# Optimization experiments

Measured on AMD Instinct MI355X. Metric: run time of the kernel, lower is better.

Reference implementation:

```python
import jax, jax.numpy as jnp
import numpy as np

B, S, D, H, E, K = 2, 1024, 768, 12, 8, 2
DF = 4 * D
HD = D // H
EPS = 1e-5

def layer_norm(x, g, b):
    m = jnp.mean(x, axis=-1, keepdims=True)
    v = jnp.mean(jnp.square(x - m), axis=-1, keepdims=True)
    return (x - m) * jax.lax.rsqrt(v + EPS) * g + b

def setup_inputs() -> dict:
    key = jax.random.key(0)
    ks = jax.random.split(key, 16)
    s = lambda i, shape, sc: jax.random.normal(ks[i], shape, jnp.float32) * sc
    return {
        'x': s(0, (B, S, D), 1.0),
        'ln1_g': jnp.ones((D,), jnp.float32), 'ln1_b': jnp.zeros((D,), jnp.float32),
        'Wq': s(1, (D, D), 0.02), 'Wk': s(2, (D, D), 0.02), 'Wv': s(3, (D, D), 0.02),
        'Wo': s(4, (D, D), 0.02), 'bo': jnp.zeros((D,), jnp.float32),
        'ln2_g': jnp.ones((D,), jnp.float32), 'ln2_b': jnp.zeros((D,), jnp.float32),
        'Wr': s(5, (D, E), 0.02), 'br': jnp.zeros((E,), jnp.float32),
        'W1': s(6, (E, D, DF), 0.02), 'b1': jnp.zeros((E, DF), jnp.float32),
        'W2': s(7, (E, DF, D), 0.02), 'b2': jnp.zeros((E, D), jnp.float32),
    }

def _attn(xn, Wq, Wk, Wv, Wo, bo):
    # xn: [B,S,D]
    q = (xn @ Wq).reshape(B, S, H, HD).transpose(0, 2, 1, 3)
    k = (xn @ Wk).reshape(B, S, H, HD).transpose(0, 2, 1, 3)
    v = (xn @ Wv).reshape(B, S, H, HD).transpose(0, 2, 1, 3)
    scores = jnp.einsum('bhqd,bhkd->bhqk', q, k) / jnp.sqrt(jnp.float32(HD))
    causal = jnp.tril(jnp.ones((S, S), bool))
    scores = jnp.where(causal, scores, jnp.float32(-1e9))
    w = jax.nn.softmax(scores, axis=-1)
    out = jnp.einsum('bhqk,bhkd->bhqd', w, v)
    out = out.transpose(0, 2, 1, 3).reshape(B, S, D)
    return out @ Wo + bo

def _smoe(xn, Wr, br, W1, b1, W2, b2):
    logits = xn @ Wr + br                               # [B,S,E]
    topv, topi = jax.lax.top_k(logits, K)               # [B,S,K]
    gw = jax.nn.softmax(topv, axis=-1)                  # softmax over selected experts
    oh = jax.nn.one_hot(topi, E, dtype=xn.dtype)        # [B,S,K,E]
    gate = jnp.einsum('bske,bsk->bse', oh, gw)          # sparse gate, zeros elsewhere
    h = jax.nn.gelu(jnp.einsum('bsd,edf->bsef', xn, W1) + b1, approximate=False)
    eo = jnp.einsum('bsef,efd->bsed', h, W2) + b2       # [B,S,E,D]
    return jnp.einsum('bsed,bse->bsd', eo, gate)

def reference(x, ln1_g, ln1_b, Wq, Wk, Wv, Wo, bo, ln2_g, ln2_b, Wr, br, W1, b1, W2, b2):
    h = x + _attn(layer_norm(x, ln1_g, ln1_b), Wq, Wk, Wv, Wo, bo)
    out = h + _smoe(layer_norm(h, ln2_g, ln2_b), Wr, br, W1, b1, W2, b2)
    return out
```

## Files before the change

### kernel.cpp

```cpp
#include <hip/hip_runtime.h>

using bf16x8 = __attribute__((ext_vector_type(8))) short;
using f32x4  = __attribute__((ext_vector_type(4))) float;

#define DEV __device__ __forceinline__

DEV short f2bf(float x){
  unsigned u = __float_as_uint(x);
  u += 0x7fffu + ((u >> 16) & 1u);
  return (short)(u >> 16);
}
DEV float bf2f(short h){ return __uint_as_float(((unsigned)(unsigned short)h) << 16); }

#define MFMA16(a,b,c) __builtin_amdgcn_mfma_f32_16x16x32_bf16(a,b,c,0,0,0)

DEV void gl_lds16(const void* g, void* l){
  __builtin_amdgcn_global_load_lds(
      (const __attribute__((address_space(1))) unsigned*)g,
      (__attribute__((address_space(3))) unsigned*)l, 16, 0, 0);
}


__global__ void k_transpose(const float* __restrict__ src, long sbatch,
                            short* __restrict__ dhi, short* __restrict__ dlo, long dbatch,
                            int R, int C){
  __shared__ float tile[32][33];
  const float* s = src + (long)blockIdx.z * sbatch;
  int c0 = blockIdx.x * 32, r0 = blockIdx.y * 32;
  int tx = threadIdx.x & 31, ty = threadIdx.x >> 5;
  #pragma unroll
  for (int i = 0; i < 4; i++)
    tile[ty + 8*i][tx] = s[(long)(r0 + ty + 8*i) * C + c0 + tx];
  __syncthreads();
  #pragma unroll
  for (int i = 0; i < 4; i++){
    int c = c0 + ty + 8*i;
    float v = tile[tx][ty + 8*i];
    short hv = f2bf(v);
    long o = (long)blockIdx.z * dbatch + (long)c * R + r0 + tx;
    dhi[o] = hv;
    if (dlo) dlo[o] = f2bf(v - bf2f(hv));
  }
}

__global__ void k_ln1(const float* __restrict__ x, const float* __restrict__ g,
                      const float* __restrict__ bb,
                      short* __restrict__ xh, short* __restrict__ xl){
  int t = blockIdx.x, tid = threadIdx.x;
  const float* xr = x + (long)t * 768;
  float v[3];
  #pragma unroll
  for (int j = 0; j < 3; j++) v[j] = xr[tid + 256*j];
  float s = v[0]+v[1]+v[2];
  float q = v[0]*v[0]+v[1]*v[1]+v[2]*v[2];
  #pragma unroll
  for (int o = 32; o > 0; o >>= 1){ s += __shfl_down(s,o,64); q += __shfl_down(q,o,64); }
  __shared__ float ss[4], qs[4];
  int w = tid >> 6;
  if ((tid & 63) == 0){ ss[w] = s; qs[w] = q; }
  __syncthreads();
  float St = ss[0]+ss[1]+ss[2]+ss[3], Qt = qs[0]+qs[1]+qs[2]+qs[3];
  float mean = St * (1.f/768.f);
  float var  = Qt * (1.f/768.f) - mean*mean;
  float inv  = 1.f / sqrtf(var + 1e-5f);
  #pragma unroll
  for (int j = 0; j < 3; j++){
    int d = tid + 256*j;
    float xn = (v[j]-mean)*inv*g[d] + bb[d];
    short hv = f2bf(xn);
    xh[(long)t*768 + d] = hv;
    xl[(long)t*768 + d] = f2bf(xn - bf2f(hv));
  }
}

__global__ __launch_bounds__(256,2) void k_qkv(
    const short* __restrict__ Ah, const short* __restrict__ Al,
    const short* __restrict__ Bh, const short* __restrict__ Bl,
    short* __restrict__ qh, short* __restrict__ ql,
    short* __restrict__ kh, short* __restrict__ kl,
    short* __restrict__ vh, short* __restrict__ vl){
  int M0 = blockIdx.x * 128, N0 = blockIdx.y * 128;
  __shared__ __align__(16) short lah[128*64], lal[128*64], lbh[128*64], lbl[128*64];
  int tid = threadIdx.x;
  int w = tid >> 6, lane = tid & 63, l15 = lane & 15, quad = lane >> 4;
  int mbase = (w & 1) * 64, nbase = (w >> 1) * 64;
  f32x4 acc[4][4];
  #pragma unroll
  for (int i = 0; i < 4; i++)
    #pragma unroll
    for (int j = 0; j < 4; j++) acc[i][j] = (f32x4){0.f,0.f,0.f,0.f};
  int rl = lane >> 3, pch = lane & 7;
  long gA[4], gB[4];
  #pragma unroll
  for (int j = 0; j < 4; j++){
    int r = w*32 + j*8 + rl;
    int c = pch ^ (r & 7);
    gA[j] = (long)(M0 + r)*768 + c*8;
    gB[j] = (long)(N0 + r)*768 + c*8;
  }
  for (int k0 = 0; k0 < 768; k0 += 64){
    #pragma unroll
    for (int j = 0; j < 4; j++){
      gl_lds16(Ah + gA[j] + k0, lah + w*2048 + j*512);
      gl_lds16(Al + gA[j] + k0, lal + w*2048 + j*512);
      gl_lds16(Bh + gB[j] + k0, lbh + w*2048 + j*512);
      gl_lds16(Bl + gB[j] + k0, lbl + w*2048 + j*512);
    }
    __syncthreads();
    #pragma unroll
    for (int kk = 0; kk < 2; kk++){
      int swq = ((kk*4 + quad) ^ (l15 & 7)) * 8;
      bf16x8 afh[4], afl[4];
      #pragma unroll
      for (int mt = 0; mt < 4; mt++){
        afh[mt] = *(const bf16x8*)&lah[(mbase+mt*16+l15)*64 + swq];
        afl[mt] = *(const bf16x8*)&lal[(mbase+mt*16+l15)*64 + swq];
      }
      #pragma unroll
      for (int nt = 0; nt < 4; nt++){
        bf16x8 bfh = *(const bf16x8*)&lbh[(nbase+nt*16+l15)*64 + swq];
        bf16x8 bfl = *(const bf16x8*)&lbl[(nbase+nt*16+l15)*64 + swq];
        #pragma unroll
        for (int mt = 0; mt < 4; mt++){
          acc[mt][nt] = MFMA16(afh[mt], bfh, acc[mt][nt]);
          acc[mt][nt] = MFMA16(afh[mt], bfl, acc[mt][nt]);
          acc[mt][nt] = MFMA16(afl[mt], bfh, acc[mt][nt]);
        }
      }
    }
    __syncthreads();
  }
  #pragma unroll
  for (int mt = 0; mt < 4; mt++){
    #pragma unroll
    for (int nt = 0; nt < 4; nt++){
      #pragma unroll
      for (int rg = 0; rg < 4; rg++){
        int m = M0 + mbase + mt*16 + quad*4 + rg;
        int n = N0 + nbase + nt*16 + l15;
        float vv = acc[mt][nt][rg];
        int bi = m >> 10, si = m & 1023;
        if (n < 768){
          float sv = vv * 0.125f;
          short hv = f2bf(sv);
          int hh = n >> 6, hd = n & 63;
          long o = (((long)(bi*12+hh)*1024) + si)*64 + hd;
          qh[o] = hv; ql[o] = f2bf(sv - bf2f(hv));
        } else if (n < 1536){
          int n2 = n - 768;
          short hv = f2bf(vv);
          int hh = n2 >> 6, hd = n2 & 63;
          long o = (((long)(bi*12+hh)*1024) + si)*64 + hd;
          kh[o] = hv; kl[o] = f2bf(vv - bf2f(hv));
        } else {
          int n2 = n - 1536;
          short hv = f2bf(vv);
          int hh = n2 >> 6, hd = n2 & 63;
          long o = (((long)(bi*12+hh)*64) + hd)*1024 + si;
          vh[o] = hv; vl[o] = f2bf(vv - bf2f(hv));
        }
      }
    }
  }
}

__global__ __launch_bounds__(256,3) void k_attn(
    const short* __restrict__ qh, const short* __restrict__ ql,
    const short* __restrict__ kh, const short* __restrict__ kl,
    const short* __restrict__ vth, const short* __restrict__ vtl,
    float* __restrict__ po, float* __restrict__ pm, float* __restrict__ pl){
  int qt = blockIdx.x >> 1, half = blockIdx.x & 1, bh = blockIdx.y;
  int q0 = qt * 64;
  long base = (long)bh * 1024 * 64;
  int ktb = half ? ((qt + 2) >> 1) : 0;
  int kte = half ? (qt + 1) : ((qt + 2) >> 1);
  __shared__ __align__(16) short skh[64*64], skl[64*64], svh[64*64], svl[64*64];
  __shared__ __align__(16) short sph[4][16*72], spl[4][16*72];
  int tid = threadIdx.x, w = tid >> 6, lane = tid & 63, l15 = lane & 15, quad = lane >> 4;
  bf16x8 qfh[2], qfl[2];
  #pragma unroll
  for (int c = 0; c < 2; c++){
    long qa = base + (long)(q0 + w*16 + l15)*64 + c*32 + quad*8;
    qfh[c] = *(const bf16x8*)(qh + qa);
    qfl[c] = *(const bf16x8*)(ql + qa);
  }
  f32x4 oacc[4];
  #pragma unroll
  for (int i = 0; i < 4; i++) oacc[i] = (f32x4){0.f,0.f,0.f,0.f};
  float m_i[4] = {-1e30f,-1e30f,-1e30f,-1e30f};
  float l_i[4] = {0.f,0.f,0.f,0.f};
  const short* gsrc = (w==0) ? kh : (w==1) ? kl : (w==2) ? vth : vtl;
  short* myb = (w==0) ? skh : (w==1) ? skl : (w==2) ? svh : svl;
  bool isv = (w >= 2);
  int rloc = lane >> 3, pch = lane & 7;
  for (int kt = ktb; kt < kte; kt++){
    #pragma unroll
    for (int j = 0; j < 8; j++){
      int r = j*8 + rloc;
      int c = pch ^ (r & 7);
      long ga = isv ? (base + (long)r*1024 + kt*64 + c*8)
                    : (base + (long)(kt*64 + r)*64 + c*8);
      gl_lds16(gsrc + ga, myb + j*512);
    }
    __syncthreads();
    f32x4 sfr[4];
    #pragma unroll
    for (int nt = 0; nt < 4; nt++){
      f32x4 c = (f32x4){0.f,0.f,0.f,0.f};
      int krow = (nt*16 + l15) * 64;
      #pragma unroll
      for (int ch = 0; ch < 2; ch++){
        int pc = ((ch*4 + quad) ^ (l15 & 7)) * 8;
        bf16x8 kfh = *(const bf16x8*)&skh[krow + pc];
        bf16x8 kfl = *(const bf16x8*)&skl[krow + pc];
        c = MFMA16(qfh[ch], kfh, c);
        c = MFMA16(qfh[ch], kfl, c);
        c = MFMA16(qfl[ch], kfh, c);
      }
      sfr[nt] = c;
    }
    if (kt == qt){
      #pragma unroll
      for (int nt = 0; nt < 4; nt++)
        #pragma unroll
        for (int rg = 0; rg < 4; rg++){
          int kp = nt*16 + l15, qp = w*16 + quad*4 + rg;
          if (kp > qp) sfr[nt][rg] = -1e30f;
        }
    }
    float rmax[4];
    #pragma unroll
    for (int rg = 0; rg < 4; rg++)
      rmax[rg] = fmaxf(fmaxf(sfr[0][rg], sfr[1][rg]), fmaxf(sfr[2][rg], sfr[3][rg]));
    #pragma unroll
    for (int xm = 1; xm < 16; xm <<= 1)
      #pragma unroll
      for (int rg = 0; rg < 4; rg++)
        rmax[rg] = fmaxf(rmax[rg], __shfl_xor(rmax[rg], xm, 64));
    float alpha[4];
    #pragma unroll
    for (int rg = 0; rg < 4; rg++){
      float mn = fmaxf(m_i[rg], rmax[rg]);
      alpha[rg] = expf(m_i[rg] - mn);
      m_i[rg] = mn;
    }
    float rsum[4] = {0.f,0.f,0.f,0.f};
    #pragma unroll
    for (int nt = 0; nt < 4; nt++)
      #pragma unroll
      for (int rg = 0; rg < 4; rg++){
        float p = expf(sfr[nt][rg] - m_i[rg]);
        sfr[nt][rg] = p; rsum[rg] += p;
      }
    #pragma unroll
    for (int xm = 1; xm < 16; xm <<= 1)
      #pragma unroll
      for (int rg = 0; rg < 4; rg++)
        rsum[rg] += __shfl_xor(rsum[rg], xm, 64);
    #pragma unroll
    for (int rg = 0; rg < 4; rg++) l_i[rg] = l_i[rg]*alpha[rg] + rsum[rg];
    #pragma unroll
    for (int hd = 0; hd < 4; hd++)
      #pragma unroll
      for (int rg = 0; rg < 4; rg++) oacc[hd][rg] *= alpha[rg];
    #pragma unroll
    for (int nt = 0; nt < 4; nt++)
      #pragma unroll
      for (int rg = 0; rg < 4; rg++){
        float p = sfr[nt][rg];
        short hv = f2bf(p);
        sph[w][(quad*4+rg)*72 + nt*16 + l15] = hv;
        spl[w][(quad*4+rg)*72 + nt*16 + l15] = f2bf(p - bf2f(hv));
      }
    bf16x8 pfh[2], pfl[2];
    #pragma unroll
    for (int ch = 0; ch < 2; ch++){
      pfh[ch] = *(const bf16x8*)&sph[w][l15*72 + ch*32 + quad*8];
      pfl[ch] = *(const bf16x8*)&spl[w][l15*72 + ch*32 + quad*8];
    }
    #pragma unroll
    for (int hd = 0; hd < 4; hd++){
      int vrow = (hd*16 + l15) * 64;
      #pragma unroll
      for (int ch = 0; ch < 2; ch++){
        int pc = ((ch*4 + quad) ^ (l15 & 7)) * 8;
        bf16x8 vfh = *(const bf16x8*)&svh[vrow + pc];
        bf16x8 vfl = *(const bf16x8*)&svl[vrow + pc];
        oacc[hd] = MFMA16(pfh[ch], vfh, oacc[hd]);
        oacc[hd] = MFMA16(pfh[ch], vfl, oacc[hd]);
        oacc[hd] = MFMA16(pfl[ch], vfh, oacc[hd]);
      }
    }
    __syncthreads();
  }
  long pb = ((long)(half*24 + bh)*1024);
  #pragma unroll
  for (int hdt = 0; hdt < 4; hdt++)
    #pragma unroll
    for (int rg = 0; rg < 4; rg++){
      int qp = q0 + w*16 + quad*4 + rg;
      po[(pb + qp)*64 + hdt*16 + l15] = oacc[hdt][rg];
    }
  if (l15 == 0){
    #pragma unroll
    for (int rg = 0; rg < 4; rg++){
      int qp = q0 + w*16 + quad*4 + rg;
      pm[pb + qp] = m_i[rg];
      pl[pb + qp] = l_i[rg];
    }
  }
}

__global__ void k_attn_combine(const float* __restrict__ po, const float* __restrict__ pm,
                               const float* __restrict__ pl,
                               short* __restrict__ oh, short* __restrict__ ol){
  int bh = blockIdx.y, tid = threadIdx.x;
  int r = blockIdx.x*64 + (tid >> 2);
  int c0 = (tid & 3) * 16;
  long i0 = (long)bh*1024 + r;
  long i1 = (long)(24 + bh)*1024 + r;
  float m0 = pm[i0], m1 = pm[i1], l0 = pl[i0], l1 = pl[i1];
  float m = fmaxf(m0, m1);
  float a0 = expf(m0 - m), a1 = expf(m1 - m);
  float inv = 1.f / (a0*l0 + a1*l1);
  a0 *= inv; a1 *= inv;
  int b = bh / 12, hh = bh % 12;
  long ob = ((long)(b*1024 + r))*768 + hh*64 + c0;
  short hv[16], lv[16];
  #pragma unroll
  for (int j = 0; j < 4; j++){
    float4 o0 = *(const float4*)&po[i0*64 + c0 + j*4];
    float4 o1 = *(const float4*)&po[i1*64 + c0 + j*4];
    float vs[4] = {a0*o0.x + a1*o1.x, a0*o0.y + a1*o1.y,
                   a0*o0.z + a1*o1.z, a0*o0.w + a1*o1.w};
    #pragma unroll
    for (int q = 0; q < 4; q++){
      short h = f2bf(vs[q]);
      hv[j*4+q] = h; lv[j*4+q] = f2bf(vs[q] - bf2f(h));
    }
  }
  *(bf16x8*)(oh + ob)     = *(bf16x8*)&hv[0];
  *(bf16x8*)(oh + ob + 8) = *(bf16x8*)&hv[8];
  *(bf16x8*)(ol + ob)     = *(bf16x8*)&lv[0];
  *(bf16x8*)(ol + ob + 8) = *(bf16x8*)&lv[8];
}

__global__ __launch_bounds__(256,2) void k_wo(
    const short* __restrict__ Ah, const short* __restrict__ Al,
    const short* __restrict__ Bh, const short* __restrict__ Bl,
    const float* __restrict__ x, const float* __restrict__ bo,
    float* __restrict__ hout){
  int M0 = blockIdx.x * 128, N0 = blockIdx.y * 128;
  __shared__ __align__(16) short lah[128*64], lal[128*64], lbh[128*64], lbl[128*64];
  int tid = threadIdx.x;
  int w = tid >> 6, lane = tid & 63, l15 = lane & 15, quad = lane >> 4;
  int mbase = (w & 1) * 64, nbase = (w >> 1) * 64;
  f32x4 acc[4][4];
  #pragma unroll
  for (int i = 0; i < 4; i++)
    #pragma unroll
    for (int j = 0; j < 4; j++) acc[i][j] = (f32x4){0.f,0.f,0.f,0.f};
  int rl = lane >> 3, pch = lane & 7;
  long gA[4], gB[4];
  #pragma unroll
  for (int j = 0; j < 4; j++){
    int r = w*32 + j*8 + rl;
    int c = pch ^ (r & 7);
    gA[j] = (long)(M0 + r)*768 + c*8;
    gB[j] = (long)(N0 + r)*768 + c*8;
  }
  for (int k0 = 0; k0 < 768; k0 += 64){
    #pragma unroll
    for (int j = 0; j < 4; j++){
      gl_lds16(Ah + gA[j] + k0, lah + w*2048 + j*512);
      gl_lds16(Al + gA[j] + k0, lal + w*2048 + j*512);
      gl_lds16(Bh + gB[j] + k0, lbh + w*2048 + j*512);
      gl_lds16(Bl + gB[j] + k0, lbl + w*2048 + j*512);
    }
    __syncthreads();
    #pragma unroll
    for (int kk = 0; kk < 2; kk++){
      int swq = ((kk*4 + quad) ^ (l15 & 7)) * 8;
      bf16x8 afh[4], afl[4];
      #pragma unroll
      for (int mt = 0; mt < 4; mt++){
        afh[mt] = *(const bf16x8*)&lah[(mbase+mt*16+l15)*64 + swq];
        afl[mt] = *(const bf16x8*)&lal[(mbase+mt*16+l15)*64 + swq];
      }
      #pragma unroll
      for (int nt = 0; nt < 4; nt++){
        bf16x8 bfh = *(const bf16x8*)&lbh[(nbase+nt*16+l15)*64 + swq];
        bf16x8 bfl = *(const bf16x8*)&lbl[(nbase+nt*16+l15)*64 + swq];
        #pragma unroll
        for (int mt = 0; mt < 4; mt++){
          acc[mt][nt] = MFMA16(afh[mt], bfh, acc[mt][nt]);
          acc[mt][nt] = MFMA16(afh[mt], bfl, acc[mt][nt]);
          acc[mt][nt] = MFMA16(afl[mt], bfh, acc[mt][nt]);
        }
      }
    }
    __syncthreads();
  }
  #pragma unroll
  for (int mt = 0; mt < 4; mt++)
    #pragma unroll
    for (int nt = 0; nt < 4; nt++)
      #pragma unroll
      for (int rg = 0; rg < 4; rg++){
        int m = M0 + mbase + mt*16 + quad*4 + rg;
        int n = N0 + nbase + nt*16 + l15;
        hout[(long)m*768 + n] = acc[mt][nt][rg] + x[(long)m*768 + n] + bo[n];
      }
}

__global__ void k_ln2router(const float* __restrict__ h, const float* __restrict__ g,
                            const float* __restrict__ bb, const float* __restrict__ Wr,
                            const float* __restrict__ br, short* __restrict__ xn2,
                            int* __restrict__ sel, float* __restrict__ gw){
  int wv = (blockIdx.x*256 + threadIdx.x) >> 6;
  int lane = threadIdx.x & 63;
  #pragma unroll
  for (int rep = 0; rep < 2; rep++){
    int t = wv*2 + rep;
    const float* xr = h + (long)t * 768;
    float v[12];
    #pragma unroll
    for (int j = 0; j < 12; j++) v[j] = xr[lane + 64*j];
    float s = 0.f, q = 0.f;
    #pragma unroll
    for (int j = 0; j < 12; j++){ s += v[j]; q += v[j]*v[j]; }
    #pragma unroll
    for (int xm = 1; xm < 64; xm <<= 1){ s += __shfl_xor(s, xm, 64); q += __shfl_xor(q, xm, 64); }
    float mean = s * (1.f/768.f);
    float var  = q * (1.f/768.f) - mean*mean;
    float inv  = 1.f / sqrtf(var + 1e-5f);
    float part[8] = {0,0,0,0,0,0,0,0};
    #pragma unroll
    for (int j = 0; j < 12; j++){
      int d = lane + 64*j;
      float xn = (v[j]-mean)*inv*g[d] + bb[d];
      xn2[(long)t*768 + d] = f2bf(xn);
      #pragma unroll
      for (int e = 0; e < 8; e++) part[e] += xn * Wr[d*8 + e];
    }
    #pragma unroll
    for (int xm = 1; xm < 64; xm <<= 1)
      #pragma unroll
      for (int e = 0; e < 8; e++) part[e] += __shfl_xor(part[e], xm, 64);
    if (lane == 0){
      float lg[8];
      #pragma unroll
      for (int e = 0; e < 8; e++) lg[e] = part[e] + br[e];
      int i1 = 0;
      for (int e = 1; e < 8; e++) if (lg[e] > lg[i1]) i1 = e;
      int i2 = -1;
      for (int e = 0; e < 8; e++){ if (e == i1) continue; if (i2 < 0 || lg[e] > lg[i2]) i2 = e; }
      float e2 = expf(lg[i2] - lg[i1]);
      float is = 1.f / (1.f + e2);
      gw[t*2]   = is;
      gw[t*2+1] = e2 * is;
      sel[t*2]   = i1;
      sel[t*2+1] = i2;
    }
  }
}

__global__ void k_build(const int* __restrict__ sel, int* __restrict__ poffs,
                        int* __restrict__ mbc, int* __restrict__ ptot,
                        int* __restrict__ pperm, int* __restrict__ inv){
  __shared__ int cnt8[8], cur[8];
  int tid = threadIdx.x;
  if (tid < 8) cnt8[tid] = 0;
  __syncthreads();
  #pragma unroll
  for (int r = 0; r < 4; r++) atomicAdd(&cnt8[sel[tid + r*1024]], 1);
  __syncthreads();
  if (tid == 0){
    int p = 0;
    for (int e = 0; e < 8; e++){
      cur[e] = p; poffs[e] = p;
      int pc = (cnt8[e] + 127) & ~127;
      mbc[e] = pc >> 7;
      p += pc;
    }
    *ptot = p;
  }
  __syncthreads();
  #pragma unroll
  for (int r = 0; r < 5; r++) pperm[tid + r*1024] = -1;
  __syncthreads();
  #pragma unroll
  for (int r = 0; r < 4; r++){
    int i = tid + r*1024;
    int pos = atomicAdd(&cur[sel[i]], 1);
    pperm[pos] = i;
    inv[i] = pos;
  }
}

__global__ __launch_bounds__(256,3) void k_moe1(
    const short* __restrict__ xn2, const short* __restrict__ W1T,
    const float* __restrict__ b1,
    const int* __restrict__ poffs, const int* __restrict__ mbc,
    const int* __restrict__ pperm, short* __restrict__ h1){
  int t = blockIdx.x;
  int e = t / 24, n = t % 24;
  if ((int)blockIdx.y >= mbc[e]) return;
  int M0 = poffs[e] + blockIdx.y * 128;
  int N0 = n * 128;
  const short* Bp = W1T + (long)e * 3072 * 768;
  __shared__ __align__(16) short la[128*64], lb[128*64];
  __shared__ int rtok[128];
  int tid = threadIdx.x, w = tid >> 6, lane = tid & 63, l15 = lane & 15, quad = lane >> 4;
  if (tid < 128) rtok[tid] = pperm[M0 + tid];
  __syncthreads();
  int rl = lane >> 3, pch = lane & 7;
  long gA[4], gB[4];
  #pragma unroll
  for (int j = 0; j < 4; j++){
    int r = w*32 + j*8 + rl;
    int c = pch ^ (r & 7);
    int tk = rtok[r]; tk = (tk >= 0) ? (tk >> 1) : 0;
    gA[j] = (long)tk*768 + c*8;
    gB[j] = (long)(N0 + r)*768 + c*8;
  }
  short* ldA = la + w*2048;
  short* ldB = lb + w*2048;
  f32x4 acc[4][4];
  #pragma unroll
  for (int i = 0; i < 4; i++)
    #pragma unroll
    for (int j = 0; j < 4; j++) acc[i][j] = (f32x4){0.f,0.f,0.f,0.f};
  int mbase = (w & 1) * 64, nbase = (w >> 1) * 64;
  for (int k0 = 0; k0 < 768; k0 += 64){
    #pragma unroll
    for (int j = 0; j < 4; j++) gl_lds16(xn2 + gA[j] + k0, ldA + j*512);
    #pragma unroll
    for (int j = 0; j < 4; j++) gl_lds16(Bp  + gB[j] + k0, ldB + j*512);
    __syncthreads();
    #pragma unroll
    for (int kk = 0; kk < 2; kk++){
      int swq = ((kk*4 + quad) ^ (l15 & 7)) * 8;
      bf16x8 af[4];
      #pragma unroll
      for (int mt = 0; mt < 4; mt++)
        af[mt] = *(const bf16x8*)&la[(mbase+mt*16+l15)*64 + swq];
      #pragma unroll
      for (int nt = 0; nt < 4; nt++){
        bf16x8 bf = *(const bf16x8*)&lb[(nbase+nt*16+l15)*64 + swq];
        #pragma unroll
        for (int mt = 0; mt < 4; mt++) acc[mt][nt] = MFMA16(af[mt], bf, acc[mt][nt]);
      }
    }
    __syncthreads();
  }
  #pragma unroll
  for (int mt = 0; mt < 4; mt++)
    #pragma unroll
    for (int nt = 0; nt < 4; nt++)
      #pragma unroll
      for (int rg = 0; rg < 4; rg++){
        int ml = mbase + mt*16 + quad*4 + rg;
        if (rtok[ml] >= 0){
          int nn = N0 + nbase + nt*16 + l15;
          float vv = acc[mt][nt][rg] + b1[e*3072 + nn];
          float gl = 0.5f * vv * (1.f + erff(vv * 0.70710678118654752f));
          h1[(long)(M0 + ml)*3072 + nn] = f2bf(gl);
        }
      }
}

__global__ __launch_bounds__(256,4) void k_moe2(
    const short* __restrict__ h1, const short* __restrict__ W2T,
    const float* __restrict__ b2,
    const int* __restrict__ poffs, const int* __restrict__ mbc,
    float* __restrict__ e0, float* __restrict__ e1,
    float* __restrict__ e2, float* __restrict__ e3){
  int t = blockIdx.x;
  int e = t / 24, r24 = t % 24;
  int n = r24 >> 2, ks = r24 & 3;
  if ((int)blockIdx.y >= mbc[e]) return;
  int M0 = poffs[e] + blockIdx.y * 128;
  int N0 = n * 128;
  int kbeg = ks * 768;
  const short* Bp = W2T + (long)e * 768 * 3072;
  float* eo = (ks == 0) ? e0 : (ks == 1) ? e1 : (ks == 2) ? e2 : e3;
  __shared__ __align__(16) short la[128*64], lb[128*64];
  int tid = threadIdx.x, w = tid >> 6, lane = tid & 63, l15 = lane & 15, quad = lane >> 4;
  int rl = lane >> 3, pch = lane & 7;
  long gA[4], gB[4];
  #pragma unroll
  for (int j = 0; j < 4; j++){
    int r = w*32 + j*8 + rl;
    int c = pch ^ (r & 7);
    gA[j] = (long)(M0 + r)*3072 + kbeg + c*8;
    gB[j] = (long)(N0 + r)*3072 + kbeg + c*8;
  }
  short* ldA = la + w*2048;
  short* ldB = lb + w*2048;
  f32x4 acc[4][4];
  #pragma unroll
  for (int i = 0; i < 4; i++)
    #pragma unroll
    for (int j = 0; j < 4; j++) acc[i][j] = (f32x4){0.f,0.f,0.f,0.f};
  int mbase = (w & 1) * 64, nbase = (w >> 1) * 64;
  for (int k0 = 0; k0 < 768; k0 += 64){
    #pragma unroll
    for (int j = 0; j < 4; j++) gl_lds16(h1 + gA[j] + k0, ldA + j*512);
    #pragma unroll
    for (int j = 0; j < 4; j++) gl_lds16(Bp + gB[j] + k0, ldB + j*512);
    __syncthreads();
    #pragma unroll
    for (int kk = 0; kk < 2; kk++){
      int swq = ((kk*4 + quad) ^ (l15 & 7)) * 8;
      bf16x8 af[4];
      #pragma unroll
      for (int mt = 0; mt < 4; mt++)
        af[mt] = *(const bf16x8*)&la[(mbase+mt*16+l15)*64 + swq];
      #pragma unroll
      for (int nt = 0; nt < 4; nt++){
        bf16x8 bf = *(const bf16x8*)&lb[(nbase+nt*16+l15)*64 + swq];
        #pragma unroll
        for (int mt = 0; mt < 4; mt++) acc[mt][nt] = MFMA16(af[mt], bf, acc[mt][nt]);
      }
    }
    __syncthreads();
  }
  #pragma unroll
  for (int mt = 0; mt < 4; mt++)
    #pragma unroll
    for (int nt = 0; nt < 4; nt++)
      #pragma unroll
      for (int rg = 0; rg < 4; rg++){
        int ml = mbase + mt*16 + quad*4 + rg;
        int nn = N0 + nbase + nt*16 + l15;
        float vv = acc[mt][nt][rg] + ((ks == 0) ? b2[e*768 + nn] : 0.f);
        eo[(long)(M0 + ml)*768 + nn] = vv;
      }
}

__global__ void k_combine(const float* __restrict__ h,
                          const float* __restrict__ e0, const float* __restrict__ e1,
                          const float* __restrict__ e2, const float* __restrict__ e3,
                          const int* __restrict__ inv, const float* __restrict__ gw,
                          float* __restrict__ out){
  int i = blockIdx.x * 256 + threadIdx.x;
  int t = i / 192, c = i - t * 192;
  int s0 = inv[2*t], s1 = inv[2*t+1];
  float g0 = gw[2*t], g1 = gw[2*t+1];
  float4 a  = ((const float4*)h)[i];
  long o0 = (long)s0*192 + c, o1 = (long)s1*192 + c;
  float4 x0 = ((const float4*)e0)[o0];
  float4 y0 = ((const float4*)e1)[o0];
  float4 z0 = ((const float4*)e2)[o0];
  float4 w0 = ((const float4*)e3)[o0];
  float4 x1 = ((const float4*)e0)[o1];
  float4 y1 = ((const float4*)e1)[o1];
  float4 z1 = ((const float4*)e2)[o1];
  float4 w1 = ((const float4*)e3)[o1];
  float4 o;
  o.x = a.x + g0*(x0.x + y0.x + z0.x + w0.x) + g1*(x1.x + y1.x + z1.x + w1.x);
  o.y = a.y + g0*(x0.y + y0.y + z0.y + w0.y) + g1*(x1.y + y1.y + z1.y + w1.y);
  o.z = a.z + g0*(x0.z + y0.z + z0.z + w0.z) + g1*(x1.z + y1.z + z1.z + w1.z);
  o.w = a.w + g0*(x0.w + y0.w + z0.w + w0.w) + g1*(x1.w + y1.w + z1.w + w1.w);
  ((float4*)out)[i] = o;
}

extern "C" void kernel_launch(void* const* d_in, const int* in_sizes, int n_in,
                              void* d_out, int out_size, void* d_ws, size_t ws_size,
                              hipStream_t stream){
  const float* x    = (const float*)d_in[0];
  const float* ln1g = (const float*)d_in[1];
  const float* ln1b = (const float*)d_in[2];
  const float* Wq   = (const float*)d_in[3];
  const float* Wk   = (const float*)d_in[4];
  const float* Wv   = (const float*)d_in[5];
  const float* Wo   = (const float*)d_in[6];
  const float* bo   = (const float*)d_in[7];
  const float* ln2g = (const float*)d_in[8];
  const float* ln2b = (const float*)d_in[9];
  const float* Wr   = (const float*)d_in[10];
  const float* br   = (const float*)d_in[11];
  const float* W1   = (const float*)d_in[12];
  const float* b1   = (const float*)d_in[13];
  const float* W2   = (const float*)d_in[14];
  const float* b2   = (const float*)d_in[15];

  char* ws = (char*)d_ws;
  size_t off = 0;
  auto alloc = [&](size_t bytes) -> void* {
    void* p = ws + off;
    off += (bytes + 255) & ~(size_t)255;
    return p;
  };
  short* WQKVH = (short*)alloc(2304l*768*2);
  short* WQKVL = (short*)alloc(2304l*768*2);
  short* WOH   = (short*)alloc(768l*768*2);
  short* WOL   = (short*)alloc(768l*768*2);
  short* W1T   = (short*)alloc(8l*3072*768*2);
  short* W2T   = (short*)alloc(8l*768*3072*2);
  short* XN1H  = (short*)alloc(2048l*768*2);
  short* XN1L  = (short*)alloc(2048l*768*2);
  short* QH    = (short*)alloc(2048l*768*2);
  short* QL    = (short*)alloc(2048l*768*2);
  short* KH    = (short*)alloc(2048l*768*2);
  short* KL    = (short*)alloc(2048l*768*2);
  short* VTH   = (short*)alloc(2048l*768*2);
  short* VTL   = (short*)alloc(2048l*768*2);
  short* ATH   = (short*)alloc(2048l*768*2);
  short* ATL   = (short*)alloc(2048l*768*2);
  float* HBUF  = (float*)alloc(2048l*768*4);
  short* XN2   = (short*)alloc(2048l*768*2);
  short* H1    = (short*)alloc(5120l*3072*2);
  float* E0    = (float*)alloc(5120l*768*4);
  float* E1    = (float*)alloc(5120l*768*4);
  float* PO    = (float*)alloc(2l*24*1024*64*4);
  float* PM    = (float*)alloc(2l*24*1024*4);
  float* PL    = (float*)alloc(2l*24*1024*4);
  int*   POFF  = (int*)alloc(8*4);
  int*   MBC   = (int*)alloc(8*4);
  int*   PTOT  = (int*)alloc(4);
  int*   SEL   = (int*)alloc(4096*4);
  int*   PPERM = (int*)alloc(5120*4);
  int*   INV   = (int*)alloc(4096*4);
  float* GW    = (float*)alloc(4096*4);
  (void)ws_size; (void)in_sizes; (void)n_in; (void)out_size;

  float* E2 = (float*)XN1H;
  float* E3 = E2 + 5120l*768;

  k_transpose<<<dim3(24,24,1),256,0,stream>>>(Wq, 0, WQKVH,             WQKVL,             0, 768, 768);
  k_transpose<<<dim3(24,24,1),256,0,stream>>>(Wk, 0, WQKVH + 768l*768,  WQKVL + 768l*768,  0, 768, 768);
  k_transpose<<<dim3(24,24,1),256,0,stream>>>(Wv, 0, WQKVH + 1536l*768, WQKVL + 1536l*768, 0, 768, 768);
  k_transpose<<<dim3(24,24,1),256,0,stream>>>(Wo, 0, WOH, WOL, 0, 768, 768);
  k_transpose<<<dim3(96,24,8),256,0,stream>>>(W1, 768l*3072, W1T, nullptr, 3072l*768, 768, 3072);
  k_transpose<<<dim3(24,96,8),256,0,stream>>>(W2, 3072l*768, W2T, nullptr, 768l*3072, 3072, 768);

  k_ln1<<<2048,256,0,stream>>>(x, ln1g, ln1b, XN1H, XN1L);
  k_qkv<<<dim3(16,18),256,0,stream>>>(XN1H, XN1L, WQKVH, WQKVL, QH, QL, KH, KL, VTH, VTL);
  k_attn<<<dim3(32,24),256,0,stream>>>(QH, QL, KH, KL, VTH, VTL, PO, PM, PL);
  k_attn_combine<<<dim3(16,24),256,0,stream>>>(PO, PM, PL, ATH, ATL);
  k_wo<<<dim3(16,6),256,0,stream>>>(ATH, ATL, WOH, WOL, x, bo, HBUF);

  k_ln2router<<<256,256,0,stream>>>(HBUF, ln2g, ln2b, Wr, br, XN2, SEL, GW);
  k_build<<<1,1024,0,stream>>>(SEL, POFF, MBC, PTOT, PPERM, INV);
  k_moe1<<<dim3(192,16),256,0,stream>>>(XN2, W1T, b1, POFF, MBC, PPERM, H1);
  k_moe2<<<dim3(192,16),256,0,stream>>>(H1, W2T, b2, POFF, MBC, E0, E1, E2, E3);
  k_combine<<<1536,256,0,stream>>>(HBUF, E0, E1, E2, E3, INV, GW, (float*)d_out);
}
```

Baseline: 465.8 us.

## Halve MoE GEMM N-tile to 64, raise occupancy, and use wave-ballot counting in k_build

Both expert GEMM kernels move from 128x128 to 128x64 output tiles, doubling the grid and raising the launch-bounds occupancy hint from 3/4 to 6 blocks per CU. The aim is to fill more CUs given the small per-expert row counts. The cost is more reloading of the A operand (tokens) per output and fewer MFMAs per LDS load. Separately, k_build replaces per-thread shared atomics with wave ballots and popcounts, which cuts atomic contention when counting tokens and assigning slots.

```diff
diff --git a/kernel.cpp b/kernel.cpp
--- a/kernel.cpp
+++ b/kernel.cpp
@@ -468,12 +468,21 @@
 __global__ void k_build(const int* __restrict__ sel, int* __restrict__ poffs,
                         int* __restrict__ mbc, int* __restrict__ ptot,
                         int* __restrict__ pperm, int* __restrict__ inv){
-  __shared__ int cnt8[8], cur[8];
+  __shared__ int cnt8[8], cur[8], wbase[16][8];
   int tid = threadIdx.x;
+  int lane = tid & 63, wv = tid >> 6;
   if (tid < 8) cnt8[tid] = 0;
   __syncthreads();
-  #pragma unroll
-  for (int r = 0; r < 4; r++) atomicAdd(&cnt8[sel[tid + r*1024]], 1);
+  int sv[4];
+  #pragma unroll
+  for (int r = 0; r < 4; r++){
+    sv[r] = sel[tid + r*1024];
+    #pragma unroll
+    for (int e = 0; e < 8; e++){
+      unsigned long long mk = __ballot(sv[r] == e);
+      if (lane == 0) atomicAdd(&cnt8[e], (int)__popcll(mk));
+    }
+  }
   __syncthreads();
   if (tid == 0){
     int p = 0;
@@ -489,54 +498,72 @@
   #pragma unroll
   for (int r = 0; r < 5; r++) pperm[tid + r*1024] = -1;
   __syncthreads();
+  unsigned long long lmask = (1ull << lane) - 1ull;
   #pragma unroll
   for (int r = 0; r < 4; r++){
+    int s = sv[r];
+    unsigned long long mk[8];
+    #pragma unroll
+    for (int e = 0; e < 8; e++) mk[e] = __ballot(s == e);
+    if (lane == 0){
+      #pragma unroll
+      for (int e = 0; e < 8; e++)
+        wbase[wv][e] = atomicAdd(&cur[e], (int)__popcll(mk[e]));
+    }
+    unsigned long long mks = 0;
+    #pragma unroll
+    for (int e = 0; e < 8; e++) if (s == e) mks = mk[e];
+    int pos = wbase[wv][s] + (int)__popcll(mks & lmask);
     int i = tid + r*1024;
-    int pos = atomicAdd(&cur[sel[i]], 1);
     pperm[pos] = i;
     inv[i] = pos;
   }
 }
 
-__global__ __launch_bounds__(256,3) void k_moe1(
+__global__ __launch_bounds__(256,6) void k_moe1(
     const short* __restrict__ xn2, const short* __restrict__ W1T,
     const float* __restrict__ b1,
     const int* __restrict__ poffs, const int* __restrict__ mbc,
     const int* __restrict__ pperm, short* __restrict__ h1){
   int t = blockIdx.x;
-  int e = t / 24, n = t % 24;
+  int e = t / 48, n = t % 48;
   if ((int)blockIdx.y >= mbc[e]) return;
   int M0 = poffs[e] + blockIdx.y * 128;
-  int N0 = n * 128;
+  int N0 = n * 64;
   const short* Bp = W1T + (long)e * 3072 * 768;
-  __shared__ __align__(16) short la[128*64], lb[128*64];
+  __shared__ __align__(16) short la[128*64], lb[64*64];
   __shared__ int rtok[128];
   int tid = threadIdx.x, w = tid >> 6, lane = tid & 63, l15 = lane & 15, quad = lane >> 4;
   if (tid < 128) rtok[tid] = pperm[M0 + tid];
   __syncthreads();
   int rl = lane >> 3, pch = lane & 7;
-  long gA[4], gB[4];
+  long gA[4], gB[2];
   #pragma unroll
   for (int j = 0; j < 4; j++){
     int r = w*32 + j*8 + rl;
     int c = pch ^ (r & 7);
     int tk = rtok[r]; tk = (tk >= 0) ? (tk >> 1) : 0;
     gA[j] = (long)tk*768 + c*8;
+  }
+  #pragma unroll
+  for (int j = 0; j < 2; j++){
+    int r = w*16 + j*8 + rl;
+    int c = pch ^ (r & 7);
     gB[j] = (long)(N0 + r)*768 + c*8;
   }
   short* ldA = la + w*2048;
-  short* ldB = lb + w*2048;
-  f32x4 acc[4][4];
+  short* ldB = lb + w*1024;
+  f32x4 acc[4][2];
   #pragma unroll
   for (int i = 0; i < 4; i++)
     #pragma unroll
-    for (int j = 0; j < 4; j++) acc[i][j] = (f32x4){0.f,0.f,0.f,0.f};
-  int mbase = (w & 1) * 64, nbase = (w >> 1) * 64;
+    for (int j = 0; j < 2; j++) acc[i][j] = (f32x4){0.f,0.f,0.f,0.f};
+  int mbase = (w & 1) * 64, nbase = (w >> 1) * 32;
   for (int k0 = 0; k0 < 768; k0 += 64){
     #pragma unroll
     for (int j = 0; j < 4; j++) gl_lds16(xn2 + gA[j] + k0, ldA + j*512);
     #pragma unroll
-    for (int j = 0; j < 4; j++) gl_lds16(Bp  + gB[j] + k0, ldB + j*512);
+    for (int j = 0; j < 2; j++) gl_lds16(Bp  + gB[j] + k0, ldB + j*512);
     __syncthreads();
     #pragma unroll
     for (int kk = 0; kk < 2; kk++){
@@ -546,7 +573,7 @@
       for (int mt = 0; mt < 4; mt++)
         af[mt] = *(const bf16x8*)&la[(mbase+mt*16+l15)*64 + swq];
       #pragma unroll
-      for (int nt = 0; nt < 4; nt++){
+      for (int nt = 0; nt < 2; nt++){
         bf16x8 bf = *(const bf16x8*)&lb[(nbase+nt*16+l15)*64 + swq];
         #pragma unroll
         for (int mt = 0; mt < 4; mt++) acc[mt][nt] = MFMA16(af[mt], bf, acc[mt][nt]);
@@ -557,7 +584,7 @@
   #pragma unroll
   for (int mt = 0; mt < 4; mt++)
     #pragma unroll
-    for (int nt = 0; nt < 4; nt++)
+    for (int nt = 0; nt < 2; nt++)
       #pragma unroll
       for (int rg = 0; rg < 4; rg++){
         int ml = mbase + mt*16 + quad*4 + rg;
@@ -570,45 +597,50 @@
       }
 }
 
-__global__ __launch_bounds__(256,4) void k_moe2(
+__global__ __launch_bounds__(256,6) void k_moe2(
     const short* __restrict__ h1, const short* __restrict__ W2T,
     const float* __restrict__ b2,
     const int* __restrict__ poffs, const int* __restrict__ mbc,
     float* __restrict__ e0, float* __restrict__ e1,
     float* __restrict__ e2, float* __restrict__ e3){
   int t = blockIdx.x;
-  int e = t / 24, r24 = t % 24;
-  int n = r24 >> 2, ks = r24 & 3;
+  int e = t / 48, r48 = t % 48;
+  int n = r48 >> 2, ks = r48 & 3;
   if ((int)blockIdx.y >= mbc[e]) return;
   int M0 = poffs[e] + blockIdx.y * 128;
-  int N0 = n * 128;
+  int N0 = n * 64;
   int kbeg = ks * 768;
   const short* Bp = W2T + (long)e * 768 * 3072;
   float* eo = (ks == 0) ? e0 : (ks == 1) ? e1 : (ks == 2) ? e2 : e3;
-  __shared__ __align__(16) short la[128*64], lb[128*64];
+  __shared__ __align__(16) short la[128*64], lb[64*64];
   int tid = threadIdx.x, w = tid >> 6, lane = tid & 63, l15 = lane & 15, quad = lane >> 4;
   int rl = lane >> 3, pch = lane & 7;
-  long gA[4], gB[4];
+  long gA[4], gB[2];
   #pragma unroll
   for (int j = 0; j < 4; j++){
     int r = w*32 + j*8 + rl;
     int c = pch ^ (r & 7);
     gA[j] = (long)(M0 + r)*3072 + kbeg + c*8;
+  }
+  #pragma unroll
+  for (int j = 0; j < 2; j++){
+    int r = w*16 + j*8 + rl;
+    int c = pch ^ (r & 7);
     gB[j] = (long)(N0 + r)*3072 + kbeg + c*8;
   }
   short* ldA = la + w*2048;
-  short* ldB = lb + w*2048;
-  f32x4 acc[4][4];
+  short* ldB = lb + w*1024;
+  f32x4 acc[4][2];
   #pragma unroll
   for (int i = 0; i < 4; i++)
     #pragma unroll
-    for (int j = 0; j < 4; j++) acc[i][j] = (f32x4){0.f,0.f,0.f,0.f};
-  int mbase = (w & 1) * 64, nbase = (w >> 1) * 64;
+    for (int j = 0; j < 2; j++) acc[i][j] = (f32x4){0.f,0.f,0.f,0.f};
+  int mbase = (w & 1) * 64, nbase = (w >> 1) * 32;
   for (int k0 = 0; k0 < 768; k0 += 64){
     #pragma unroll
     for (int j = 0; j < 4; j++) gl_lds16(h1 + gA[j] + k0, ldA + j*512);
     #pragma unroll
-    for (int j = 0; j < 4; j++) gl_lds16(Bp + gB[j] + k0, ldB + j*512);
+    for (int j = 0; j < 2; j++) gl_lds16(Bp + gB[j] + k0, ldB + j*512);
     __syncthreads();
     #pragma unroll
     for (int kk = 0; kk < 2; kk++){
@@ -618,7 +650,7 @@
       for (int mt = 0; mt < 4; mt++)
         af[mt] = *(const bf16x8*)&la[(mbase+mt*16+l15)*64 + swq];
       #pragma unroll
-      for (int nt = 0; nt < 4; nt++){
+      for (int nt = 0; nt < 2; nt++){
         bf16x8 bf = *(const bf16x8*)&lb[(nbase+nt*16+l15)*64 + swq];
         #pragma unroll
         for (int mt = 0; mt < 4; mt++) acc[mt][nt] = MFMA16(af[mt], bf, acc[mt][nt]);
@@ -629,7 +661,7 @@
   #pragma unroll
   for (int mt = 0; mt < 4; mt++)
     #pragma unroll
-    for (int nt = 0; nt < 4; nt++)
+    for (int nt = 0; nt < 2; nt++)
       #pragma unroll
       for (int rg = 0; rg < 4; rg++){
         int ml = mbase + mt*16 + quad*4 + rg;
@@ -744,7 +776,7 @@
 
   k_ln2router<<<256,256,0,stream>>>(HBUF, ln2g, ln2b, Wr, br, XN2, SEL, GW);
   k_build<<<1,1024,0,stream>>>(SEL, POFF, MBC, PTOT, PPERM, INV);
-  k_moe1<<<dim3(192,16),256,0,stream>>>(XN2, W1T, b1, POFF, MBC, PPERM, H1);
-  k_moe2<<<dim3(192,16),256,0,stream>>>(H1, W2T, b2, POFF, MBC, E0, E1, E2, E3);
+  k_moe1<<<dim3(384,16),256,0,stream>>>(XN2, W1T, b1, POFF, MBC, PPERM, H1);
+  k_moe2<<<dim3(384,16),256,0,stream>>>(H1, W2T, b2, POFF, MBC, E0, E1, E2, E3);
   k_combine<<<1536,256,0,stream>>>(HBUF, E0, E1, E2, E3, INV, GW, (float*)d_out);
 }
```

After: 479.7 us. +3.0%, slower.

## Double-buffer LDS tiles in MoE GEMMs and use wave ballots in expert bucketing

Applied to the files above, without the earlier changes.

Both MoE GEMM kernels now keep two LDS buffers and prefetch the next K-slice with global_load_lds while computing on the current one, so memory latency can overlap with MFMA work. Launch bounds drop to 2 blocks per CU to make room for the doubled shared memory. The expert bucketing kernel replaces per-thread LDS atomics with wave-level ballot and popcount, issuing one atomic per expert per wave. The lower occupancy and the extra LDS may offset part of the overlap gain.

```diff
diff --git a/kernel.cpp b/kernel.cpp
--- a/kernel.cpp
+++ b/kernel.cpp
@@ -468,12 +468,21 @@
 __global__ void k_build(const int* __restrict__ sel, int* __restrict__ poffs,
                         int* __restrict__ mbc, int* __restrict__ ptot,
                         int* __restrict__ pperm, int* __restrict__ inv){
-  __shared__ int cnt8[8], cur[8];
+  __shared__ int cnt8[8], cur[8], wbase[16][8];
   int tid = threadIdx.x;
+  int lane = tid & 63, wv = tid >> 6;
   if (tid < 8) cnt8[tid] = 0;
   __syncthreads();
-  #pragma unroll
-  for (int r = 0; r < 4; r++) atomicAdd(&cnt8[sel[tid + r*1024]], 1);
+  int sv[4];
+  #pragma unroll
+  for (int r = 0; r < 4; r++){
+    sv[r] = sel[tid + r*1024];
+    #pragma unroll
+    for (int e = 0; e < 8; e++){
+      unsigned long long mk = __ballot(sv[r] == e);
+      if (lane == 0) atomicAdd(&cnt8[e], (int)__popcll(mk));
+    }
+  }
   __syncthreads();
   if (tid == 0){
     int p = 0;
@@ -489,16 +498,29 @@
   #pragma unroll
   for (int r = 0; r < 5; r++) pperm[tid + r*1024] = -1;
   __syncthreads();
+  unsigned long long lmask = (1ull << lane) - 1ull;
   #pragma unroll
   for (int r = 0; r < 4; r++){
+    int s = sv[r];
+    unsigned long long mk[8];
+    #pragma unroll
+    for (int e = 0; e < 8; e++) mk[e] = __ballot(s == e);
+    if (lane == 0){
+      #pragma unroll
+      for (int e = 0; e < 8; e++)
+        wbase[wv][e] = atomicAdd(&cur[e], (int)__popcll(mk[e]));
+    }
+    unsigned long long mks = 0;
+    #pragma unroll
+    for (int e = 0; e < 8; e++) if (s == e) mks = mk[e];
+    int pos = wbase[wv][s] + (int)__popcll(mks & lmask);
     int i = tid + r*1024;
-    int pos = atomicAdd(&cur[sel[i]], 1);
     pperm[pos] = i;
     inv[i] = pos;
   }
 }
 
-__global__ __launch_bounds__(256,3) void k_moe1(
+__global__ __launch_bounds__(256,2) void k_moe1(
     const short* __restrict__ xn2, const short* __restrict__ W1T,
     const float* __restrict__ b1,
     const int* __restrict__ poffs, const int* __restrict__ mbc,
@@ -509,7 +531,7 @@
   int M0 = poffs[e] + blockIdx.y * 128;
   int N0 = n * 128;
   const short* Bp = W1T + (long)e * 3072 * 768;
-  __shared__ __align__(16) short la[128*64], lb[128*64];
+  __shared__ __align__(16) short la[2][128*64], lb[2][128*64];
   __shared__ int rtok[128];
   int tid = threadIdx.x, w = tid >> 6, lane = tid & 63, l15 = lane & 15, quad = lane >> 4;
   if (tid < 128) rtok[tid] = pperm[M0 + tid];
@@ -524,30 +546,37 @@
     gA[j] = (long)tk*768 + c*8;
     gB[j] = (long)(N0 + r)*768 + c*8;
   }
-  short* ldA = la + w*2048;
-  short* ldB = lb + w*2048;
   f32x4 acc[4][4];
   #pragma unroll
   for (int i = 0; i < 4; i++)
     #pragma unroll
     for (int j = 0; j < 4; j++) acc[i][j] = (f32x4){0.f,0.f,0.f,0.f};
   int mbase = (w & 1) * 64, nbase = (w >> 1) * 64;
+  #pragma unroll
+  for (int j = 0; j < 4; j++){
+    gl_lds16(xn2 + gA[j], &la[0][w*2048 + j*512]);
+    gl_lds16(Bp  + gB[j], &lb[0][w*2048 + j*512]);
+  }
+  __syncthreads();
   for (int k0 = 0; k0 < 768; k0 += 64){
-    #pragma unroll
-    for (int j = 0; j < 4; j++) gl_lds16(xn2 + gA[j] + k0, ldA + j*512);
-    #pragma unroll
-    for (int j = 0; j < 4; j++) gl_lds16(Bp  + gB[j] + k0, ldB + j*512);
-    __syncthreads();
+    int cur = (k0 >> 6) & 1;
+    if (k0 + 64 < 768){
+      #pragma unroll
+      for (int j = 0; j < 4; j++){
+        gl_lds16(xn2 + gA[j] + k0 + 64, &la[cur^1][w*2048 + j*512]);
+        gl_lds16(Bp  + gB[j] + k0 + 64, &lb[cur^1][w*2048 + j*512]);
+      }
+    }
     #pragma unroll
     for (int kk = 0; kk < 2; kk++){
       int swq = ((kk*4 + quad) ^ (l15 & 7)) * 8;
       bf16x8 af[4];
       #pragma unroll
       for (int mt = 0; mt < 4; mt++)
-        af[mt] = *(const bf16x8*)&la[(mbase+mt*16+l15)*64 + swq];
+        af[mt] = *(const bf16x8*)&la[cur][(mbase+mt*16+l15)*64 + swq];
       #pragma unroll
       for (int nt = 0; nt < 4; nt++){
-        bf16x8 bf = *(const bf16x8*)&lb[(nbase+nt*16+l15)*64 + swq];
+        bf16x8 bf = *(const bf16x8*)&lb[cur][(nbase+nt*16+l15)*64 + swq];
         #pragma unroll
         for (int mt = 0; mt < 4; mt++) acc[mt][nt] = MFMA16(af[mt], bf, acc[mt][nt]);
       }
@@ -570,7 +599,7 @@
       }
 }
 
-__global__ __launch_bounds__(256,4) void k_moe2(
+__global__ __launch_bounds__(256,2) void k_moe2(
     const short* __restrict__ h1, const short* __restrict__ W2T,
     const float* __restrict__ b2,
     const int* __restrict__ poffs, const int* __restrict__ mbc,
@@ -585,7 +614,7 @@
   int kbeg = ks * 768;
   const short* Bp = W2T + (long)e * 768 * 3072;
   float* eo = (ks == 0) ? e0 : (ks == 1) ? e1 : (ks == 2) ? e2 : e3;
-  __shared__ __align__(16) short la[128*64], lb[128*64];
+  __shared__ __align__(16) short la[2][128*64], lb[2][128*64];
   int tid = threadIdx.x, w = tid >> 6, lane = tid & 63, l15 = lane & 15, quad = lane >> 4;
   int rl = lane >> 3, pch = lane & 7;
   long gA[4], gB[4];
@@ -596,30 +625,37 @@
     gA[j] = (long)(M0 + r)*3072 + kbeg + c*8;
     gB[j] = (long)(N0 + r)*3072 + kbeg + c*8;
   }
-  short* ldA = la + w*2048;
-  short* ldB = lb + w*2048;
   f32x4 acc[4][4];
   #pragma unroll
   for (int i = 0; i < 4; i++)
     #pragma unroll
     for (int j = 0; j < 4; j++) acc[i][j] = (f32x4){0.f,0.f,0.f,0.f};
   int mbase = (w & 1) * 64, nbase = (w >> 1) * 64;
+  #pragma unroll
+  for (int j = 0; j < 4; j++){
+    gl_lds16(h1 + gA[j], &la[0][w*2048 + j*512]);
+    gl_lds16(Bp + gB[j], &lb[0][w*2048 + j*512]);
+  }
+  __syncthreads();
   for (int k0 = 0; k0 < 768; k0 += 64){
-    #pragma unroll
-    for (int j = 0; j < 4; j++) gl_lds16(h1 + gA[j] + k0, ldA + j*512);
-    #pragma unroll
-    for (int j = 0; j < 4; j++) gl_lds16(Bp + gB[j] + k0, ldB + j*512);
-    __syncthreads();
+    int cur = (k0 >> 6) & 1;
+    if (k0 + 64 < 768){
+      #pragma unroll
+      for (int j = 0; j < 4; j++){
+        gl_lds16(h1 + gA[j] + k0 + 64, &la[cur^1][w*2048 + j*512]);
+        gl_lds16(Bp + gB[j] + k0 + 64, &lb[cur^1][w*2048 + j*512]);
+      }
+    }
     #pragma unroll
     for (int kk = 0; kk < 2; kk++){
       int swq = ((kk*4 + quad) ^ (l15 & 7)) * 8;
       bf16x8 af[4];
       #pragma unroll
       for (int mt = 0; mt < 4; mt++)
-        af[mt] = *(const bf16x8*)&la[(mbase+mt*16+l15)*64 + swq];
+        af[mt] = *(const bf16x8*)&la[cur][(mbase+mt*16+l15)*64 + swq];
       #pragma unroll
       for (int nt = 0; nt < 4; nt++){
-        bf16x8 bf = *(const bf16x8*)&lb[(nbase+nt*16+l15)*64 + swq];
+        bf16x8 bf = *(const bf16x8*)&lb[cur][(nbase+nt*16+l15)*64 + swq];
         #pragma unroll
         for (int mt = 0; mt < 4; mt++) acc[mt][nt] = MFMA16(af[mt], bf, acc[mt][nt]);
       }
```

Result: slower. 504.7 us (+8.4%).
